# Optimization experiments

Measured on AMD Instinct MI355X. Metric: run time of the kernel, lower is better.

The kernel has to match this reference:

```python
import jax, jax.numpy as jnp
import numpy as np

B, S, HID = 1, 2048, 4096
NH, NKV, HD = 32, 8, 128
INIT, RECENT, HEAVY = 128, 512, 512
THETA = 10000.0


def _rope(x, pos):
    # x: [B,H,S,D]; standard Llama rotary embedding (rotate_half convention)
    d = x.shape[-1]
    inv = 1.0 / (THETA ** (jnp.arange(0, d, 2, dtype=jnp.float32) / d))
    ang = pos[:, None] * inv[None, :]                      # [S, D/2]
    cos = jnp.concatenate([jnp.cos(ang), jnp.cos(ang)], -1)  # [S, D]
    sin = jnp.concatenate([jnp.sin(ang), jnp.sin(ang)], -1)
    x1, x2 = x[..., : d // 2], x[..., d // 2:]
    rot = jnp.concatenate([-x2, x1], -1)
    return x * cos + rot * sin


def setup_inputs() -> dict:
    key = jax.random.key(0)
    ks = jax.random.split(key, 5)
    s = 1.0 / np.sqrt(HID)
    return {
        "hidden_states": jax.random.normal(ks[0], (B, S, HID), jnp.float32),
        "wq": jax.random.normal(ks[1], (HID, NH * HD), jnp.float32) * s,
        "wk": jax.random.normal(ks[2], (HID, NKV * HD), jnp.float32) * s,
        "wv": jax.random.normal(ks[3], (HID, NKV * HD), jnp.float32) * s,
        "wo": jax.random.normal(ks[4], (NH * HD, HID), jnp.float32) * s,
    }


def reference(hidden_states, wq, wk, wv, wo):
    # QKV projections (no bias, per attention_bias=False)
    q = (hidden_states @ wq).reshape(B, S, NH, HD).transpose(0, 2, 1, 3)   # [B,NH,S,D]
    k = (hidden_states @ wk).reshape(B, S, NKV, HD).transpose(0, 2, 1, 3)  # [B,NKV,S,D]
    v = (hidden_states @ wv).reshape(B, S, NKV, HD).transpose(0, 2, 1, 3)
    pos = jnp.arange(S, dtype=jnp.float32)
    q = _rope(q, pos)
    k = _rope(k, pos)
    # repeat_kv for GQA
    rep = NH // NKV
    k = jnp.repeat(k, rep, axis=1)
    v = jnp.repeat(v, rep, axis=1)

    scores = jnp.einsum('bhqd,bhkd->bhqk', q, k) / np.sqrt(HD)  # [B,NH,S,S]

    qi = jnp.arange(S)[:, None]
    ki = jnp.arange(S)[None, :]
    causal = ki <= qi
    # causal_heavy_recent_mask: tril(diag = k - q - recent) with [:, :init] = False
    middle = (ki <= qi - RECENT) & (ki >= INIT)   # heavy-hitter eligible region
    base = causal & jnp.logical_not(middle)       # init + recent tokens always kept

    neg = jnp.finfo(scores.dtype).min
    mid_scores = jnp.where(middle[None, None], scores, neg)
    _, idx = jax.lax.top_k(mid_scores, HEAVY)     # [B,NH,S,HEAVY]
    flat = idx.reshape(-1, HEAVY)
    rows = jnp.arange(flat.shape[0])[:, None]
    heavy = jnp.zeros((flat.shape[0], S), dtype=bool).at[rows, flat].set(True)
    heavy = heavy.reshape(B, NH, S, S) & middle[None, None]

    mask = base[None, None] | heavy
    attn = jax.nn.softmax(jnp.where(mask, scores, neg), axis=-1)
    out = jnp.einsum('bhqk,bhkd->bhqd', attn, v)
    out = out.transpose(0, 2, 1, 3).reshape(B, S, NH * HD)
    return out @ wo
```

## Files before the change

kernel.cpp:

```cpp
#include <hip/hip_runtime.h>
#include <math.h>

#define S_LEN 2048
#define HID_N 4096
#define NH 32
#define NKV 8
#define HD 128
#define INIT_N 128
#define RECENT_N 512
#define HEAVY_N 512
#define SCALE_QK 0.08838834764831845f

typedef __attribute__((ext_vector_type(8))) short short8;
typedef __attribute__((ext_vector_type(4))) float float4v;

__device__ __forceinline__ unsigned short f2bf(float f) {
  unsigned u = __float_as_uint(f);
  unsigned r = (u + 0x7FFFu + ((u >> 16) & 1u)) >> 16;
  return (unsigned short)r;
}

__device__ __forceinline__ float bf2f(unsigned u) { return __uint_as_float(u << 16); }

__device__ __forceinline__ unsigned fkey16(unsigned u) {
  return (u & 0x8000u) ? ((~u) & 0xFFFFu) : (u | 0x8000u);
}

__device__ __forceinline__ void gld_lds16(const unsigned short* g, unsigned short* l) {
  __builtin_amdgcn_global_load_lds(
      (const __attribute__((address_space(1))) unsigned int*)g,
      (__attribute__((address_space(3))) unsigned int*)l, 16, 0, 0);
}

__global__ __launch_bounds__(256) void cast_bf16x8(const float* __restrict__ x,
                                                   unsigned short* __restrict__ y, int n) {
  int i = (blockIdx.x * 256 + threadIdx.x) << 3;
  if (i >= n) return;
  float4 a = *(const float4*)(x + i);
  float4 b = *(const float4*)(x + i + 4);
  union { unsigned short u[8]; short8 v; } o;
  o.u[0] = f2bf(a.x); o.u[1] = f2bf(a.y); o.u[2] = f2bf(a.z); o.u[3] = f2bf(a.w);
  o.u[4] = f2bf(b.x); o.u[5] = f2bf(b.y); o.u[6] = f2bf(b.z); o.u[7] = f2bf(b.w);
  *(short8*)(y + i) = o.v;
}

__global__ __launch_bounds__(256) void transpose_cast(const float* __restrict__ w,
                                                      unsigned short* __restrict__ wt,
                                                      int R, int C, int ldw) {
  __shared__ unsigned short t[64][65];
  const int c0 = blockIdx.x * 64;
  const int r0 = blockIdx.y * 64;
  const int tx = threadIdx.x & 63;
  const int ty = threadIdx.x >> 6;
#pragma unroll
  for (int i = 0; i < 16; ++i)
    t[ty + 4 * i][tx] = f2bf(w[(size_t)(r0 + ty + 4 * i) * ldw + c0 + tx]);
  __syncthreads();
#pragma unroll
  for (int i = 0; i < 16; ++i)
    wt[(size_t)(c0 + ty + 4 * i) * R + r0 + tx] = t[tx][ty + 4 * i];
}

__global__ __launch_bounds__(256) void gemm_bf16(const unsigned short* __restrict__ A,
                                                 const unsigned short* __restrict__ BT,
                                                 float* __restrict__ C,
                                                 int M, int N, int K) {
  __shared__ __align__(16) unsigned short As[128 * 32];
  __shared__ __align__(16) unsigned short Bs[128 * 32];
  const int tid = threadIdx.x;
  const int lane = tid & 63;
  const int wid = tid >> 6;
  const int m0 = blockIdx.y * 128;
  const int n0 = blockIdx.x * 128;
  const int wm = (wid & 1) * 64;
  const int wn = (wid >> 1) * 64;
  const int col = lane & 15;
  const int quad = lane >> 4;

  float4v acc[4][4] = {};

  const int crow = tid >> 2;
  const int ckc = (tid & 3) << 3;

  for (int k0 = 0; k0 < K; k0 += 32) {
#pragma unroll
    for (int i = 0; i < 2; ++i) {
      const int row = i * 64 + crow;
      unsigned short* la = &As[(i * 256 + wid * 64) << 3];
      unsigned short* lb = &Bs[(i * 256 + wid * 64) << 3];
      gld_lds16(A + (size_t)(m0 + row) * K + k0 + ckc, la);
      gld_lds16(BT + (size_t)(n0 + row) * K + k0 + ckc, lb);
    }
    __syncthreads();

    short8 af[4], bf[4];
#pragma unroll
    for (int i = 0; i < 4; ++i) {
      af[i] = *(const short8*)&As[((wm + 16 * i + col) << 5) + (quad << 3)];
      bf[i] = *(const short8*)&Bs[((wn + 16 * i + col) << 5) + (quad << 3)];
    }
#pragma unroll
    for (int i = 0; i < 4; ++i)
#pragma unroll
      for (int j = 0; j < 4; ++j)
        acc[i][j] = __builtin_amdgcn_mfma_f32_16x16x32_bf16(af[i], bf[j], acc[i][j], 0, 0, 0);
    __syncthreads();
  }

#pragma unroll
  for (int i = 0; i < 4; ++i)
#pragma unroll
    for (int j = 0; j < 4; ++j) {
      size_t base = (size_t)(m0 + wm + 16 * i + quad * 4) * N + n0 + wn + 16 * j + col;
      C[base] = acc[i][j][0];
      C[base + N] = acc[i][j][1];
      C[base + 2 * (size_t)N] = acc[i][j][2];
      C[base + 3 * (size_t)N] = acc[i][j][3];
    }
}

__global__ __launch_bounds__(256) void rope_cast(const float* __restrict__ x,
                                                 unsigned short* __restrict__ y,
                                                 int nheads, int ldx, int ldy) {
  int idx = blockIdx.x * 256 + threadIdx.x;
  int i = idx & 63;
  int rest = idx >> 6;
  int hh = rest % nheads;
  int s = rest / nheads;
  if (s >= S_LEN) return;
  const float* p = x + (size_t)s * ldx + hh * HD;
  unsigned short* o = y + (size_t)s * ldy + hh * HD;
  float inv = (float)(1.0 / pow(10000.0, (double)(2 * i) / 128.0));
  float ang = (float)s * inv;
  float c = cosf(ang);
  float sn = sinf(ang);
  float x1 = p[i];
  float x2 = p[i + 64];
  o[i] = f2bf(x1 * c - x2 * sn);
  o[i + 64] = f2bf(x2 * c + x1 * sn);
}

template <int SMAX>
__global__ __launch_bounds__(256, SMAX == 1024 ? 4 : 2)
void attn_mfma(const unsigned short* __restrict__ qb,
               const unsigned short* __restrict__ kb,
               const unsigned short* __restrict__ vt,
               unsigned short* __restrict__ ao16, int qbase) {
  const int qi0 = (qbase + blockIdx.x) << 4;
  const int h = blockIdx.y;
  const int g = h >> 2;
  const int tid = threadIdx.x;
  const int lane = tid & 63;
  const int wid = tid >> 6;
  const int col = lane & 15;
  const int quad = lane >> 4;
  const int nkm = qi0 + 16;
  const int nkm32 = (nkm + 31) & ~31;

  __shared__ __align__(16) unsigned short sc[16 * SMAX];
  __shared__ float sumv[16];

  short8 qf[4];
  {
    const unsigned short* qrow = qb + (size_t)(qi0 + col) * (NH * HD) + h * HD + (quad << 3);
#pragma unroll
    for (int dt = 0; dt < 4; ++dt) qf[dt] = *(const short8*)(qrow + dt * 32);
  }
  const int ntiles = nkm >> 4;
  int t = wid;
  for (; t + 4 < ntiles; t += 8) {
    const int k0a = t << 4;
    const int k0b = (t + 4) << 4;
    const unsigned short* kra = kb + (size_t)(k0a + col) * (NKV * HD) + g * HD + (quad << 3);
    const unsigned short* krb = kb + (size_t)(k0b + col) * (NKV * HD) + g * HD + (quad << 3);
    short8 kfa[4], kfb[4];
#pragma unroll
    for (int dt = 0; dt < 4; ++dt) kfa[dt] = *(const short8*)(kra + dt * 32);
#pragma unroll
    for (int dt = 0; dt < 4; ++dt) kfb[dt] = *(const short8*)(krb + dt * 32);
    float4v acca = {}, accb = {};
#pragma unroll
    for (int dt = 0; dt < 4; ++dt) {
      acca = __builtin_amdgcn_mfma_f32_16x16x32_bf16(qf[dt], kfa[dt], acca, 0, 0, 0);
      accb = __builtin_amdgcn_mfma_f32_16x16x32_bf16(qf[dt], kfb[dt], accb, 0, 0, 0);
    }
#pragma unroll
    for (int r = 0; r < 4; ++r) {
      int q = (quad << 2) + r;
      sc[(q * SMAX + k0a + col) ^ ((q & 7) << 3)] = f2bf(acca[r] * SCALE_QK);
      sc[(q * SMAX + k0b + col) ^ ((q & 7) << 3)] = f2bf(accb[r] * SCALE_QK);
    }
  }
  if (t < ntiles) {
    const int k0 = t << 4;
    const unsigned short* krow = kb + (size_t)(k0 + col) * (NKV * HD) + g * HD + (quad << 3);
    float4v acc = {};
#pragma unroll
    for (int dt = 0; dt < 4; ++dt) {
      short8 kf = *(const short8*)(krow + dt * 32);
      acc = __builtin_amdgcn_mfma_f32_16x16x32_bf16(qf[dt], kf, acc, 0, 0, 0);
    }
#pragma unroll
    for (int r = 0; r < 4; ++r) {
      int q = (quad << 2) + r;
      sc[(q * SMAX + k0 + col) ^ ((q & 7) << 3)] = f2bf(acc[r] * SCALE_QK);
    }
  }
  __syncthreads();

  const unsigned long long lmlt = (1ull << lane) - 1ull;
  for (int rr = 0; rr < 4; ++rr) {
    const int r = (wid << 2) + rr;
    const int qi = qi0 + r;
    const int mhi = qi - RECENT_N;
    const int m = mhi - INIT_N + 1;
    const bool need = (SMAX > 1024) && (m > HEAVY_N);
    const unsigned swz = (r & 7) << 3;
    const int rbase = r * SMAX;

    unsigned T = 0, rem = 0;
    if (need) {
      unsigned myk[22];
#pragma unroll
      for (int j = 0; j < 11; ++j) {
        int off = (lane + (j << 6)) << 1;
        unsigned u = *(const unsigned*)&sc[(rbase + INIT_N + off) ^ swz];
        unsigned f0 = fkey16(u & 0xFFFFu);
        unsigned f1 = fkey16(u >> 16);
        myk[2 * j] = (off < m) ? f0 : 0u;
        myk[2 * j + 1] = (off + 1 < m) ? f1 : 0u;
      }
      unsigned prefix = 0, rm = HEAVY_N;
#pragma unroll 1
      for (int bit = 15; bit >= 0; --bit) {
        unsigned target = (prefix >> bit) | 1u;
        unsigned cnt = 0;
#pragma unroll
        for (int j = 0; j < 22; ++j)
          cnt += (unsigned)__popcll(__ballot((myk[j] >> bit) == target));
        if (cnt >= rm) prefix |= (1u << bit);
        else rm -= cnt;
      }
      T = prefix;
      rem = rm;
    }

    float mx = -3.402823466e38f;
#pragma unroll 1
    for (int c0 = 0; c0 <= qi; c0 += 128) {
      int k2 = c0 + (lane << 1);
      unsigned u = *(const unsigned*)&sc[(rbase + k2) ^ swz];
      float s0 = bf2f(u & 0xFFFFu);
      float s1 = bf2f(u >> 16);
      if (k2 <= qi) mx = fmaxf(mx, s0);
      if (k2 + 1 <= qi) mx = fmaxf(mx, s1);
    }
#pragma unroll
    for (int off = 32; off; off >>= 1) mx = fmaxf(mx, __shfl_xor(mx, off, 64));

    float sum = 0.f;
    unsigned cum = 0;
#pragma unroll 1
    for (int c0 = 0; c0 < nkm32; c0 += 128) {
      int k2 = c0 + (lane << 1);
      int idx = (rbase + k2) ^ swz;
      unsigned u = *(const unsigned*)&sc[idx];
      bool ic0 = k2 <= qi, ic1 = (k2 + 1) <= qi;
      bool sel0, sel1;
      if (!need) {
        sel0 = ic0;
        sel1 = ic1;
      } else {
        bool mid0 = ic0 && (k2 >= INIT_N) && (k2 <= mhi);
        bool mid1 = ic1 && (k2 + 1 >= INIT_N) && (k2 + 1 <= mhi);
        unsigned f0 = fkey16(u & 0xFFFFu);
        unsigned f1 = fkey16(u >> 16);
        unsigned long long eq0 = __ballot(mid0 && (f0 == T));
        unsigned long long eq1 = __ballot(mid1 && (f1 == T));
        unsigned pre0 = cum + (unsigned)__popcll(eq0 & lmlt) + (unsigned)__popcll(eq1 & lmlt);
        unsigned pre1 = pre0 + (unsigned)((eq0 >> lane) & 1ull);
        sel0 = ic0 && (!mid0 || (f0 > T) || ((f0 == T) && (pre0 < rem)));
        sel1 = ic1 && (!mid1 || (f1 > T) || ((f1 == T) && (pre1 < rem)));
        cum += (unsigned)__popcll(eq0) + (unsigned)__popcll(eq1);
      }
      float e0 = sel0 ? __expf(bf2f(u & 0xFFFFu) - mx) : 0.f;
      float e1 = sel1 ? __expf(bf2f(u >> 16) - mx) : 0.f;
      sum += e0 + e1;
      *(unsigned*)&sc[idx] = (unsigned)f2bf(e0) | ((unsigned)f2bf(e1) << 16);
    }
#pragma unroll
    for (int off = 32; off; off >>= 1) sum += __shfl_xor(sum, off, 64);
    if (lane == 0) sumv[r] = sum;
  }
  __syncthreads();

  float4v a0 = {}, a1 = {}, b0 = {}, b1 = {};
  const int db = wid << 5;
  const unsigned short* vrow0 = vt + (size_t)(g * HD + db + col) * S_LEN + (quad << 3);
  const unsigned short* vrow1 = vrow0 + (size_t)16 * S_LEN;
  const unsigned pswz = (unsigned)((col & 7) << 3);
  int k0 = 0;
  for (; k0 + 32 < nkm32; k0 += 64) {
    short8 pf0 = *(const short8*)&sc[(col * SMAX + k0 + (quad << 3)) ^ pswz];
    short8 pf1 = *(const short8*)&sc[(col * SMAX + k0 + 32 + (quad << 3)) ^ pswz];
    short8 v00 = *(const short8*)(vrow0 + k0);
    short8 v01 = *(const short8*)(vrow1 + k0);
    short8 v10 = *(const short8*)(vrow0 + k0 + 32);
    short8 v11 = *(const short8*)(vrow1 + k0 + 32);
    a0 = __builtin_amdgcn_mfma_f32_16x16x32_bf16(pf0, v00, a0, 0, 0, 0);
    a1 = __builtin_amdgcn_mfma_f32_16x16x32_bf16(pf0, v01, a1, 0, 0, 0);
    b0 = __builtin_amdgcn_mfma_f32_16x16x32_bf16(pf1, v10, b0, 0, 0, 0);
    b1 = __builtin_amdgcn_mfma_f32_16x16x32_bf16(pf1, v11, b1, 0, 0, 0);
  }
  if (k0 < nkm32) {
    short8 pf = *(const short8*)&sc[(col * SMAX + k0 + (quad << 3)) ^ pswz];
    short8 v0 = *(const short8*)(vrow0 + k0);
    short8 v1 = *(const short8*)(vrow1 + k0);
    a0 = __builtin_amdgcn_mfma_f32_16x16x32_bf16(pf, v0, a0, 0, 0, 0);
    a1 = __builtin_amdgcn_mfma_f32_16x16x32_bf16(pf, v1, a1, 0, 0, 0);
  }
  a0 += b0;
  a1 += b1;
#pragma unroll
  for (int r = 0; r < 4; ++r) {
    int qq = (quad << 2) + r;
    float inv = 1.0f / sumv[qq];
    size_t o = (size_t)(qi0 + qq) * (NH * HD) + h * HD + db;
    ao16[o + col] = f2bf(a0[r] * inv);
    ao16[o + 16 + col] = f2bf(a1[r] * inv);
  }
}

extern "C" void kernel_launch(void* const* d_in, const int* in_sizes, int n_in,
                              void* d_out, int out_size, void* d_ws, size_t ws_size,
                              hipStream_t stream) {
  const float* hidden = (const float*)d_in[0];
  const float* wq = (const float*)d_in[1];
  const float* wk = (const float*)d_in[2];
  const float* wv = (const float*)d_in[3];
  const float* wo = (const float*)d_in[4];
  float* out = (float*)d_out;

  float* ws = (float*)d_ws;
  const size_t M1 = 1024 * 1024;
  float* qkv = ws;
  unsigned short* qb16 = (unsigned short*)(ws + 12 * M1);
  unsigned short* hb = (unsigned short*)(ws + 16 * M1);
  unsigned short* aob = hb;
  unsigned short* wqkvT = (unsigned short*)(ws + 20 * M1);
  unsigned short* woT = wqkvT;
  unsigned short* kb16 = (unsigned short*)(ws + 28 * M1);
  unsigned short* vT16 = (unsigned short*)(ws + 29 * M1);

  dim3 blk(256);
  const int NE = S_LEN * HID_N;

  cast_bf16x8<<<NE / 2048, blk, 0, stream>>>(hidden, hb, NE);
  transpose_cast<<<dim3(HID_N / 64, HID_N / 64), blk, 0, stream>>>(wq, wqkvT, HID_N, HID_N, HID_N);
  transpose_cast<<<dim3((NKV * HD) / 64, HID_N / 64), blk, 0, stream>>>(
      wk, wqkvT + (size_t)HID_N * HID_N, HID_N, NKV * HD, NKV * HD);
  transpose_cast<<<dim3((NKV * HD) / 64, HID_N / 64), blk, 0, stream>>>(
      wv, wqkvT + (size_t)(HID_N + NKV * HD) * HID_N, HID_N, NKV * HD, NKV * HD);

  gemm_bf16<<<dim3(6144 / 128, S_LEN / 128), blk, 0, stream>>>(hb, wqkvT, qkv, S_LEN, 6144, HID_N);

  transpose_cast<<<dim3(HID_N / 64, HID_N / 64), blk, 0, stream>>>(wo, woT, NH * HD, HID_N, HID_N);

  rope_cast<<<(S_LEN * NH * 64) / 256, blk, 0, stream>>>(qkv, qb16, NH, 6144, NH * HD);
  rope_cast<<<(S_LEN * NKV * 64) / 256, blk, 0, stream>>>(qkv + HID_N, kb16, NKV, 6144, NKV * HD);
  transpose_cast<<<dim3((NKV * HD) / 64, S_LEN / 64), blk, 0, stream>>>(
      qkv + HID_N + NKV * HD, vT16, S_LEN, NKV * HD, 6144);

  attn_mfma<2048><<<dim3(64, NH), blk, 0, stream>>>(qb16, kb16, vT16, aob, 64);
  attn_mfma<1024><<<dim3(64, NH), blk, 0, stream>>>(qb16, kb16, vT16, aob, 0);

  gemm_bf16<<<dim3(HID_N / 128, S_LEN / 128), blk, 0, stream>>>(aob, woT, out, S_LEN, HID_N, NH * HD);
}
```

Baseline: 941.9 us.

## Use 512-thread blocks in attention kernel with work split across eight waves

Doubles the attention block from four to eight waves. QK tiles are strided by 8/16, each wave handles two query rows in the heavy-hitter top-k and softmax stage instead of four, and each wave computes a 16-wide slice of the head dimension in the PV stage. The goal is more parallelism per 16-query tile and a shorter serial per-row selection loop. In exchange, launch bounds change to 512 threads with a different occupancy hint, which may raise register pressure and lower the number of resident blocks.

```diff
diff --git a/kernel.cpp b/kernel.cpp
--- a/kernel.cpp
+++ b/kernel.cpp
@@ -141,7 +141,7 @@
 }
 
 template <int SMAX>
-__global__ __launch_bounds__(256, SMAX == 1024 ? 4 : 2)
+__global__ __launch_bounds__(512, 4)
 void attn_mfma(const unsigned short* __restrict__ qb,
                const unsigned short* __restrict__ kb,
                const unsigned short* __restrict__ vt,
@@ -168,9 +168,9 @@
   }
   const int ntiles = nkm >> 4;
   int t = wid;
-  for (; t + 4 < ntiles; t += 8) {
+  for (; t + 8 < ntiles; t += 16) {
     const int k0a = t << 4;
-    const int k0b = (t + 4) << 4;
+    const int k0b = (t + 8) << 4;
     const unsigned short* kra = kb + (size_t)(k0a + col) * (NKV * HD) + g * HD + (quad << 3);
     const unsigned short* krb = kb + (size_t)(k0b + col) * (NKV * HD) + g * HD + (quad << 3);
     short8 kfa[4], kfb[4];
@@ -209,8 +209,9 @@
   __syncthreads();
 
   const unsigned long long lmlt = (1ull << lane) - 1ull;
-  for (int rr = 0; rr < 4; ++rr) {
-    const int r = (wid << 2) + rr;
+#pragma unroll 1
+  for (int rr = 0; rr < 2; ++rr) {
+    const int r = (wid << 1) + rr;
     const int qi = qi0 + r;
     const int mhi = qi - RECENT_N;
     const int m = mhi - INIT_N + 1;
@@ -294,40 +295,31 @@
   }
   __syncthreads();
 
-  float4v a0 = {}, a1 = {}, b0 = {}, b1 = {};
-  const int db = wid << 5;
-  const unsigned short* vrow0 = vt + (size_t)(g * HD + db + col) * S_LEN + (quad << 3);
-  const unsigned short* vrow1 = vrow0 + (size_t)16 * S_LEN;
+  float4v a0 = {}, b0 = {};
+  const int db = wid << 4;
+  const unsigned short* vrow = vt + (size_t)(g * HD + db + col) * S_LEN + (quad << 3);
   const unsigned pswz = (unsigned)((col & 7) << 3);
   int k0 = 0;
   for (; k0 + 32 < nkm32; k0 += 64) {
     short8 pf0 = *(const short8*)&sc[(col * SMAX + k0 + (quad << 3)) ^ pswz];
     short8 pf1 = *(const short8*)&sc[(col * SMAX + k0 + 32 + (quad << 3)) ^ pswz];
-    short8 v00 = *(const short8*)(vrow0 + k0);
-    short8 v01 = *(const short8*)(vrow1 + k0);
-    short8 v10 = *(const short8*)(vrow0 + k0 + 32);
-    short8 v11 = *(const short8*)(vrow1 + k0 + 32);
-    a0 = __builtin_amdgcn_mfma_f32_16x16x32_bf16(pf0, v00, a0, 0, 0, 0);
-    a1 = __builtin_amdgcn_mfma_f32_16x16x32_bf16(pf0, v01, a1, 0, 0, 0);
-    b0 = __builtin_amdgcn_mfma_f32_16x16x32_bf16(pf1, v10, b0, 0, 0, 0);
-    b1 = __builtin_amdgcn_mfma_f32_16x16x32_bf16(pf1, v11, b1, 0, 0, 0);
+    short8 v0 = *(const short8*)(vrow + k0);
+    short8 v1 = *(const short8*)(vrow + k0 + 32);
+    a0 = __builtin_amdgcn_mfma_f32_16x16x32_bf16(pf0, v0, a0, 0, 0, 0);
+    b0 = __builtin_amdgcn_mfma_f32_16x16x32_bf16(pf1, v1, b0, 0, 0, 0);
   }
   if (k0 < nkm32) {
     short8 pf = *(const short8*)&sc[(col * SMAX + k0 + (quad << 3)) ^ pswz];
-    short8 v0 = *(const short8*)(vrow0 + k0);
-    short8 v1 = *(const short8*)(vrow1 + k0);
+    short8 v0 = *(const short8*)(vrow + k0);
     a0 = __builtin_amdgcn_mfma_f32_16x16x32_bf16(pf, v0, a0, 0, 0, 0);
-    a1 = __builtin_amdgcn_mfma_f32_16x16x32_bf16(pf, v1, a1, 0, 0, 0);
   }
   a0 += b0;
-  a1 += b1;
 #pragma unroll
   for (int r = 0; r < 4; ++r) {
     int qq = (quad << 2) + r;
     float inv = 1.0f / sumv[qq];
     size_t o = (size_t)(qi0 + qq) * (NH * HD) + h * HD + db;
     ao16[o + col] = f2bf(a0[r] * inv);
-    ao16[o + 16 + col] = f2bf(a1[r] * inv);
   }
 }
 
@@ -371,8 +363,8 @@
   transpose_cast<<<dim3((NKV * HD) / 64, S_LEN / 64), blk, 0, stream>>>(
       qkv + HID_N + NKV * HD, vT16, S_LEN, NKV * HD, 6144);
 
-  attn_mfma<2048><<<dim3(64, NH), blk, 0, stream>>>(qb16, kb16, vT16, aob, 64);
-  attn_mfma<1024><<<dim3(64, NH), blk, 0, stream>>>(qb16, kb16, vT16, aob, 0);
+  attn_mfma<2048><<<dim3(64, NH), dim3(512), 0, stream>>>(qb16, kb16, vT16, aob, 64);
+  attn_mfma<1024><<<dim3(64, NH), dim3(512), 0, stream>>>(qb16, kb16, vT16, aob, 0);
 
   gemm_bf16<<<dim3(HID_N / 128, S_LEN / 128), blk, 0, stream>>>(aob, woT, out, S_LEN, HID_N, NH * HD);
 }
```

Result: faster. 850.9 us (-9.7%).
